# Optimization experiments

Hardware: AMD Instinct MI355X
Metric: run time of the kernel (lower is better)

## Reference

```python
import jax, jax.numpy as jnp
import numpy as np

NUM_HEADS = 4
HEAD_DIM = 64
IN_CH = 192
KERNEL_SIZES = (3, 5, 7, 9)  # per-head neighborhood size
NEG_INF = -1e30


def setup_inputs() -> dict:
    key = jax.random.key(0)
    k1, k2, k3 = jax.random.split(key, 3)
    x = jax.random.normal(k1, (8, IN_CH, 96, 96), dtype=jnp.float32)
    # QKV conv: out_channels = head_dim * num_heads * 3 = 768, 3x3, pad 1
    w_qkv = jax.random.normal(k2, (HEAD_DIM * NUM_HEADS * 3, IN_CH, 3, 3), dtype=jnp.float32) * 0.02
    b_qkv = jax.random.normal(k3, (HEAD_DIM * NUM_HEADS * 3,), dtype=jnp.float32) * 0.02
    return {"x": x, "w_qkv": w_qkv, "b_qkv": b_qkv}


def _neighborhood_attention(q, k, v, ksize):
    # q, k, v: [N, H, W, D]; KxK zero-padded neighborhood attention with
    # out-of-bounds positions masked out.
    N, H, W, D = q.shape
    pad = ksize // 2
    kp = jnp.pad(k, ((0, 0), (pad, pad), (pad, pad), (0, 0)))
    vp = jnp.pad(v, ((0, 0), (pad, pad), (pad, pad), (0, 0)))
    scale = 1.0 / np.sqrt(D).astype(np.float32)
    rows = jnp.arange(H)
    cols = jnp.arange(W)
    scores, masks = [], []
    for di in range(ksize):
        for dj in range(ksize):
            k_sh = kp[:, di:di + H, dj:dj + W, :]           # shifted keys
            scores.append(jnp.einsum('nhwd,nhwd->nhw', q, k_sh))
            rv = (rows + di - pad >= 0) & (rows + di - pad < H)   # [H]
            cv = (cols + dj - pad >= 0) & (cols + dj - pad < W)   # [W]
            masks.append(rv[:, None] & cv[None, :])               # [H, W]
    scores = jnp.stack(scores, axis=-1) * scale                   # [N,H,W,K2]
    mask = jnp.stack(masks, axis=-1)[None]                        # [1,H,W,K2]
    scores = jnp.where(mask, scores, NEG_INF)
    attn = jax.nn.softmax(scores, axis=-1)                        # [N,H,W,K2]
    out = jnp.zeros_like(q)
    t = 0
    for di in range(ksize):
        for dj in range(ksize):
            out = out + attn[..., t, None] * vp[:, di:di + H, dj:dj + W, :]
            t += 1
    return out  # [N,H,W,D]


def reference(x, w_qkv, b_qkv):
    # Dense QKV projection (Conv2d, stride 1, padding 1 == SAME for k=3)
    qkv = jax.lax.conv_general_dilated(
        x, w_qkv, window_strides=(1, 1), padding='SAME',
        dimension_numbers=('NCHW', 'OIHW', 'NCHW'))
    qkv = qkv + b_qkv[None, :, None, None]
    # transform_to_nhw1c: NCHW -> NHWC, then split channels into
    # num_heads blocks of 3*head_dim, each split into q, k, v.
    N, C, H, W = qkv.shape
    qkv = jnp.transpose(qkv, (0, 2, 3, 1)).reshape(N, H, W, NUM_HEADS, 3, HEAD_DIM)
    outs = []
    for h, ks in enumerate(KERNEL_SIZES):
        q = qkv[..., h, 0, :]
        k = qkv[..., h, 1, :]
        v = qkv[..., h, 2, :]
        o = _neighborhood_attention(q, k, v, ks)       # [N,H,W,D]
        outs.append(jnp.transpose(o, (0, 3, 1, 2)))    # transform_from_nhw1c -> NCHW
    return jnp.stack(outs, axis=0)  # [num_heads, N, D, H, W]
```

## Files before the change

kernel.cpp:

```cpp
#include <hip/hip_runtime.h>
#include <hip/hip_bf16.h>

#define NH 96
#define NW 96
#define NB 8
#define CIN 192
#define COUT 768
#define PH 98

typedef __attribute__((ext_vector_type(8))) unsigned short ushort8;
typedef __attribute__((ext_vector_type(8))) short bf16x8;
typedef __attribute__((ext_vector_type(4))) float f32x4;

static __device__ __forceinline__ unsigned short f2bf(float f) {
    unsigned int u = __float_as_uint(f);
    return (unsigned short)((u + 0x7fffu + ((u >> 16) & 1u)) >> 16);
}

typedef const __attribute__((address_space(1))) unsigned int gu32;
typedef __attribute__((address_space(3))) unsigned int lu32;
static __device__ __forceinline__ void gload16(const void* g, void* l) {
    __builtin_amdgcn_global_load_lds((gu32*)g, (lu32*)l, 16, 0, 0);
}

__global__ __launch_bounds__(256) void pack_x_kernel(
    const float* __restrict__ x, unsigned short* __restrict__ xp)
{
    __shared__ float tile[32][97];
    int bid = blockIdx.x;
    int ct = bid % 6; int y = (bid / 6) % NH; int n = bid / (6 * NH);
    int tid = threadIdx.x;
    int c0 = ct * 32;
    for (int i = tid; i < 32 * 96; i += 256) {
        int c = i / 96, xx = i % 96;
        tile[c][xx] = x[(((size_t)n * CIN + c0 + c) * NH + y) * NW + xx];
    }
    __syncthreads();
    for (int i = tid; i < 96 * 4; i += 256) {
        int xx = i >> 2, ch = i & 3;
        ushort8 pk;
#pragma unroll
        for (int j = 0; j < 8; ++j) pk[j] = f2bf(tile[ch * 8 + j][xx]);
        *(ushort8*)(xp + ((size_t)(n * PH + y + 1) * PH + xx + 1) * CIN + c0 + ch * 8) = pk;
    }
}

__global__ __launch_bounds__(256) void pack_w_kernel(
    const float* __restrict__ w, unsigned short* __restrict__ bw)
{
    __shared__ float ls[1728];
    int co = blockIdx.x; int tid = threadIdx.x;
    for (int i = tid; i < 1728; i += 256) ls[i] = w[(size_t)co * 1728 + i];
    __syncthreads();
    for (int i = tid; i < 1728; i += 256) {
        int sh = i / 192, ci = i % 192;
        bw[(size_t)co * 1728 + i] = f2bf(ls[ci * 9 + sh]);
    }
}

#define STAGE(S, BUF)                                                          \
    {                                                                          \
        int shift_ = (S) / 6, kk_ = (S) - shift_ * 6;                          \
        int aO_ = ((shift_ / 3) * PH + (shift_ % 3)) * CIN + kk_ * 32;         \
        int bO_ = (S) * 32;                                                    \
        _Pragma("unroll")                                                      \
        for (int i_ = 0; i_ < 2; ++i_) {                                       \
            gload16(srcA[i_] + aO_, dstA[i_] + (BUF));                         \
            gload16(srcB[i_] + bO_, dstB[i_] + (BUF));                         \
        }                                                                      \
    }

#define COMPUTE(CUR)                                                           \
    {                                                                          \
        bf16x8 af[8], bf[4];                                                   \
        _Pragma("unroll")                                                      \
        for (int m_ = 0; m_ < 8; ++m_)                                         \
            af[m_] = *(const bf16x8*)(smem + (CUR) + aoff[m_]);                \
        _Pragma("unroll")                                                      \
        for (int n_ = 0; n_ < 4; ++n_)                                         \
            bf[n_] = *(const bf16x8*)(smem + (CUR) + boff[n_]);                \
        __builtin_amdgcn_s_setprio(1);                                         \
        _Pragma("unroll")                                                      \
        for (int m_ = 0; m_ < 8; ++m_)                                         \
            _Pragma("unroll")                                                  \
            for (int n_ = 0; n_ < 4; ++n_)                                     \
                acc[m_][n_] = __builtin_amdgcn_mfma_f32_16x16x32_bf16(         \
                    af[m_], bf[n_], acc[m_][n_], 0, 0, 0);                     \
        __builtin_amdgcn_s_setprio(0);                                         \
    }

__global__ __launch_bounds__(512, 2) void conv_gemm_kernel(
    const unsigned short* __restrict__ xp, const unsigned short* __restrict__ bw,
    const float* __restrict__ bias, unsigned short* __restrict__ qkq,
    unsigned short* __restrict__ vt)
{
    __shared__ __align__(16) char smem[131072];
    int bid = (blockIdx.x & 7) * 108 + (blockIdx.x >> 3);
    int brow = (bid / 3) * 256, bcol = (bid % 3) * 256;
    int tid = threadIdx.x, lane = tid & 63, wid = tid >> 6;
    int wm = wid >> 2, wn = wid & 3;

    const unsigned short* srcA[2];
    const unsigned short* srcB[2];
    char* dstA[2];
    char* dstB[2];
#pragma unroll
    for (int i = 0; i < 2; ++i) {
        int s = i * 512 + tid;
        int row = s >> 2, c = s & 3;
        int p = brow + row;
        int n = p / 9216; int rem = p - n * 9216;
        int y = rem / 96; int xx = rem - y * 96;
        int csw = (c ^ ((row >> 1) & 3)) << 3;
        srcA[i] = xp + ((size_t)(n * PH + y) * PH + xx) * CIN + csw;
        srcB[i] = bw + (size_t)(bcol + row) * 1728 + csw;
        int uslot = i * 512 + (tid & ~63);
        dstA[i] = smem + uslot * 16;
        dstB[i] = smem + 16384 + uslot * 16;
    }

    int aoff[8], boff[4];
#pragma unroll
    for (int m = 0; m < 8; ++m) {
        int rowA = wm * 128 + m * 16 + (lane & 15);
        aoff[m] = rowA * 64 + (((lane >> 4) ^ ((rowA >> 1) & 3)) << 4);
    }
#pragma unroll
    for (int n = 0; n < 4; ++n) {
        int colB = wn * 64 + n * 16 + (lane & 15);
        boff[n] = 16384 + colB * 64 + (((lane >> 4) ^ ((colB >> 1) & 3)) << 4);
    }

    STAGE(0, 0);
    STAGE(1, 32768);
    STAGE(2, 65536);

    f32x4 acc[8][4] = {};

    for (int t = 0; t < 52; ++t) {
        asm volatile("s_waitcnt vmcnt(8)" ::: "memory");
        __builtin_amdgcn_s_barrier();
        if (t < 51) STAGE(t + 3, ((t + 3) & 3) << 15);
        __builtin_amdgcn_sched_barrier(0);
        COMPUTE((t & 3) << 15);
    }
    asm volatile("s_waitcnt vmcnt(4)" ::: "memory");
    __builtin_amdgcn_s_barrier();
    COMPUTE((52 & 3) << 15);
    asm volatile("s_waitcnt vmcnt(0)" ::: "memory");
    __builtin_amdgcn_s_barrier();
    COMPUTE((53 & 3) << 15);

    __syncthreads();
    unsigned short* sc = (unsigned short*)smem;
    float bn[4];
#pragma unroll
    for (int n = 0; n < 4; ++n)
        bn[n] = bias[bcol + wn * 64 + n * 16 + (lane & 15)];
#pragma unroll
    for (int m = 0; m < 8; ++m)
#pragma unroll
        for (int n = 0; n < 4; ++n) {
            int col = wn * 64 + n * 16 + (lane & 15);
            int cabs = bcol + col;
            float scale = ((cabs % 192) < 64) ? 0.125f : 1.0f;
#pragma unroll
            for (int j = 0; j < 4; ++j) {
                int row = wm * 128 + m * 16 + (lane >> 4) * 4 + j;
                sc[row * 256 + (col ^ ((row & 7) << 3))] =
                    f2bf((acc[m][n][j] + bn[n]) * scale);
            }
        }
    __syncthreads();
#pragma unroll
    for (int i = 0; i < 16; ++i) {
        int idx = i * 512 + tid;
        int row = idx >> 5, ch = idx & 31;
        int c0 = bcol + ch * 8;
        int r192 = c0 % 192;
        if (r192 < 128) {
            ushort8 pk = *(const ushort8*)(sc + row * 256 + ((ch * 8) ^ ((row & 7) << 3)));
            *(ushort8*)(qkq + (size_t)(brow + row) * 512 + (c0 / 192) * 128 + r192) = pk;
        }
    }
    int nblk = brow / 9216;
    int prem = brow - nblk * 9216;
#pragma unroll
    for (int h = 0; h < 4; ++h) {
        int lc = h * 192 + 128 - bcol;
        if (lc < 0 || lc > 192) continue;
        unsigned short* vth = vt + (size_t)h * 4718592;
#pragma unroll
        for (int it = 0; it < 4; ++it) {
            int i = it * 512 + tid;
            int d = i & 63, pxb = i >> 6;
            ushort8 pk;
#pragma unroll
            for (int j = 0; j < 8; ++j) {
                int px = pxb * 8 + j;
                pk[j] = sc[px * 256 + ((lc + d) ^ ((px & 7) << 3))];
            }
            *(ushort8*)(vth + ((size_t)(nblk * 64 + d)) * 9216 + prem + pxb * 8) = pk;
        }
    }
}

template<int KS>
static __device__ __forceinline__ void na_body(
    const unsigned short* __restrict__ qkq, const unsigned short* __restrict__ vt,
    float* __restrict__ out, int head, int bid)
{
    constexpr int PAD = KS / 2;
    __shared__ float sO[64][97];
    int y = bid % 96, n = bid / 96;
    int tid = threadIdx.x;
    int wv = tid >> 6, lane = tid & 63;
    int g = lane >> 4, pix = lane & 15;
    int x0 = wv * 16;
    int x = x0 + pix;
    int W = x0 - 8;

    size_t qbase = ((size_t)((n * 96 + y) * 96 + x)) * 512 + (size_t)head * 128;
    bf16x8 qf0 = *(const bf16x8*)(qkq + qbase + g * 8);
    bf16x8 qf1 = *(const bf16x8*)(qkq + qbase + 32 + g * 8);

    f32x4 s[KS][2];
#pragma unroll
    for (int di = 0; di < KS; ++di)
#pragma unroll
        for (int kt = 0; kt < 2; ++kt)
#pragma unroll
            for (int r = 0; r < 4; ++r) s[di][kt][r] = -1e30f;

#pragma unroll
    for (int di = 0; di < KS; ++di) {
        int iy = y + di - PAD;
        if (iy < 0 || iy >= 96) continue;
#pragma unroll
        for (int kt = 0; kt < 2; ++kt) {
            int kix_l = W + kt * 16 + pix;
            int ixc = min(max(kix_l, 0), 95);
            size_t kbase = ((size_t)((n * 96 + iy) * 96 + ixc)) * 512
                           + (size_t)head * 128 + 64;
            bf16x8 kf0 = *(const bf16x8*)(qkq + kbase + g * 8);
            bf16x8 kf1 = *(const bf16x8*)(qkq + kbase + 32 + g * 8);
            f32x4 t = {};
            t = __builtin_amdgcn_mfma_f32_16x16x32_bf16(kf0, qf0, t, 0, 0, 0);
            t = __builtin_amdgcn_mfma_f32_16x16x32_bf16(kf1, qf1, t, 0, 0, 0);
#pragma unroll
            for (int r = 0; r < 4; ++r) {
                int kix = W + kt * 16 + g * 4 + r;
                bool valid = ((unsigned)(kix - x + PAD) <= (unsigned)(2 * PAD)) &&
                             ((unsigned)kix < 96u);
                s[di][kt][r] = valid ? t[r] : -1e30f;
            }
        }
    }

    float m = -3.0e38f;
#pragma unroll
    for (int di = 0; di < KS; ++di)
#pragma unroll
        for (int kt = 0; kt < 2; ++kt)
#pragma unroll
            for (int r = 0; r < 4; ++r) m = fmaxf(m, s[di][kt][r]);
    m = fmaxf(m, __shfl_xor(m, 16, 64));
    m = fmaxf(m, __shfl_xor(m, 32, 64));
    float l = 0.f;
#pragma unroll
    for (int di = 0; di < KS; ++di)
#pragma unroll
        for (int kt = 0; kt < 2; ++kt)
#pragma unroll
            for (int r = 0; r < 4; ++r) {
                float p = __expf(s[di][kt][r] - m);
                s[di][kt][r] = p;
                l += p;
            }
    l += __shfl_xor(l, 16, 64);
    l += __shfl_xor(l, 32, 64);

    f32x4 O[4] = {};
    int addrA = ((2 * (g & 1)) * 16 + pix) * 4;
    int addrB = addrA + 64;
    bool kthi = (g >> 1) != 0;
#pragma unroll
    for (int di = 0; di < KS; ++di) {
        int iy = y + di - PAD;
        if (iy < 0 || iy >= 96) continue;
        unsigned int w0[2], w1[2];
#pragma unroll
        for (int kt = 0; kt < 2; ++kt) {
            asm("v_cvt_pk_bf16_f32 %0, %1, %2"
                : "=v"(w0[kt]) : "v"(s[di][kt][0]), "v"(s[di][kt][1]));
            asm("v_cvt_pk_bf16_f32 %0, %1, %2"
                : "=v"(w1[kt]) : "v"(s[di][kt][2]), "v"(s[di][kt][3]));
        }
        int a0 = __builtin_amdgcn_ds_bpermute(addrA, (int)w0[0]);
        int b0 = __builtin_amdgcn_ds_bpermute(addrA, (int)w0[1]);
        int a1 = __builtin_amdgcn_ds_bpermute(addrA, (int)w1[0]);
        int b1 = __builtin_amdgcn_ds_bpermute(addrA, (int)w1[1]);
        int a2 = __builtin_amdgcn_ds_bpermute(addrB, (int)w0[0]);
        int b2 = __builtin_amdgcn_ds_bpermute(addrB, (int)w0[1]);
        int a3 = __builtin_amdgcn_ds_bpermute(addrB, (int)w1[0]);
        int b3 = __builtin_amdgcn_ds_bpermute(addrB, (int)w1[1]);
        union { int u[4]; bf16x8 v; } pa;
        pa.u[0] = kthi ? b0 : a0;
        pa.u[1] = kthi ? b1 : a1;
        pa.u[2] = kthi ? b2 : a2;
        pa.u[3] = kthi ? b3 : a3;
#pragma unroll
        for (int dc = 0; dc < 4; ++dc) {
            long voff = ((long)((n * 64 + dc * 16 + pix) * 96 + iy)) * 96 + (W + g * 8);
            bf16x8 vf = *(const bf16x8*)(vt + voff);
            O[dc] = __builtin_amdgcn_mfma_f32_16x16x32_bf16(pa.v, vf, O[dc], 0, 0, 0);
        }
    }

    float linv = 1.0f / l;
    float linvj[4];
#pragma unroll
    for (int j = 0; j < 4; ++j)
        linvj[j] = __uint_as_float((unsigned)__builtin_amdgcn_ds_bpermute(
            (4 * g + j) * 4, (int)__float_as_uint(linv)));
#pragma unroll
    for (int dc = 0; dc < 4; ++dc)
#pragma unroll
        for (int j = 0; j < 4; ++j)
            sO[dc * 16 + pix][x0 + g * 4 + j] = O[dc][j] * linvj[j];
    __syncthreads();
    for (int i = tid; i < 1536; i += 384) {
        int d = i / 24, xq = i % 24;
        float4 v4 = { sO[d][xq * 4], sO[d][xq * 4 + 1],
                      sO[d][xq * 4 + 2], sO[d][xq * 4 + 3] };
        *(float4*)(out + ((size_t)(head * 8 + n) * 64 + d) * 9216
                   + y * 96 + xq * 4) = v4;
    }
}

__global__ __launch_bounds__(384, 3) void na_mfma_all(
    const unsigned short* __restrict__ qkq, const unsigned short* __restrict__ vt,
    float* __restrict__ out)
{
    int head = blockIdx.x / 768;
    int bid = blockIdx.x % 768;
    switch (head) {
        case 0: na_body<3>(qkq, vt,               out, 0, bid); break;
        case 1: na_body<5>(qkq, vt + 4718592,     out, 1, bid); break;
        case 2: na_body<7>(qkq, vt + 2 * 4718592, out, 2, bid); break;
        default: na_body<9>(qkq, vt + 3 * 4718592, out, 3, bid); break;
    }
}

extern "C" void kernel_launch(void* const* d_in, const int* in_sizes, int n_in,
                              void* d_out, int out_size, void* d_ws, size_t ws_size,
                              hipStream_t stream) {
    const float* x  = (const float*)d_in[0];
    const float* w  = (const float*)d_in[1];
    const float* b  = (const float*)d_in[2];
    float* out = (float*)d_out;

    unsigned short* qkq  = (unsigned short*)d_ws;
    unsigned short* vt   = (unsigned short*)((char*)d_ws + 75497472);
    unsigned short* xpad = (unsigned short*)((char*)d_ws + 113246208);
    unsigned short* bw   = (unsigned short*)((char*)d_ws + 142749696);

    hipMemsetAsync(xpad, 0, 29503488, stream);
    pack_x_kernel<<<NB * NH * 6, 256, 0, stream>>>(x, xpad);
    pack_w_kernel<<<COUT, 256, 0, stream>>>(w, bw);
    conv_gemm_kernel<<<864, 512, 0, stream>>>(xpad, bw, b, qkq, vt);

    na_mfma_all<<<4 * 768, 384, 0, stream>>>(qkq, vt, out);
}
```

Before: 373.5 us.

## Interleave LDS reads, global prefetch and MFMA in two phases per k-step

Splits the GEMM main loop body into two halves. Each half issues LDS fragment reads and half of the next stage's global_load_lds copies, then runs MFMAs under raised wave priority (s_setprio), with barriers separating the phases. The aim is to keep memory traffic and matrix-core work overlapped across waves in a ping-pong schedule. It adds extra barriers per iteration, which may cost synchronisation time if the waves do not settle into alternating phases.

```diff
diff --git a/kernel.cpp b/kernel.cpp
--- a/kernel.cpp
+++ b/kernel.cpp
@@ -140,9 +140,51 @@
     for (int t = 0; t < 52; ++t) {
         asm volatile("s_waitcnt vmcnt(8)" ::: "memory");
         __builtin_amdgcn_s_barrier();
-        if (t < 51) STAGE(t + 3, ((t + 3) & 3) << 15);
-        __builtin_amdgcn_sched_barrier(0);
-        COMPUTE((t & 3) << 15);
+        const int cur = (t & 3) << 15;
+        bf16x8 af[8], bf[4];
+#pragma unroll
+        for (int m_ = 0; m_ < 4; ++m_) af[m_] = *(const bf16x8*)(smem + cur + aoff[m_]);
+#pragma unroll
+        for (int n_ = 0; n_ < 4; ++n_) bf[n_] = *(const bf16x8*)(smem + cur + boff[n_]);
+        if (t < 51) {
+            int S = t + 3, BUF = (S & 3) << 15;
+            int shift_ = S / 6, kk_ = S - shift_ * 6;
+            int aO_ = ((shift_ / 3) * PH + (shift_ % 3)) * CIN + kk_ * 32;
+            gload16(srcA[0] + aO_, dstA[0] + BUF);
+            gload16(srcA[1] + aO_, dstA[1] + BUF);
+        }
+        asm volatile("" ::: "memory");
+        __builtin_amdgcn_s_barrier();
+        __builtin_amdgcn_s_setprio(1);
+#pragma unroll
+        for (int m_ = 0; m_ < 4; ++m_)
+#pragma unroll
+            for (int n_ = 0; n_ < 4; ++n_)
+                acc[m_][n_] = __builtin_amdgcn_mfma_f32_16x16x32_bf16(
+                    af[m_], bf[n_], acc[m_][n_], 0, 0, 0);
+        __builtin_amdgcn_s_setprio(0);
+        asm volatile("" ::: "memory");
+        __builtin_amdgcn_s_barrier();
+#pragma unroll
+        for (int m_ = 4; m_ < 8; ++m_) af[m_] = *(const bf16x8*)(smem + cur + aoff[m_]);
+        if (t < 51) {
+            int S = t + 3, BUF = (S & 3) << 15;
+            int bO_ = S * 32;
+            gload16(srcB[0] + bO_, dstB[0] + BUF);
+            gload16(srcB[1] + bO_, dstB[1] + BUF);
+        }
+        asm volatile("" ::: "memory");
+        __builtin_amdgcn_s_barrier();
+        __builtin_amdgcn_s_setprio(1);
+#pragma unroll
+        for (int m_ = 4; m_ < 8; ++m_)
+#pragma unroll
+            for (int n_ = 0; n_ < 4; ++n_)
+                acc[m_][n_] = __builtin_amdgcn_mfma_f32_16x16x32_bf16(
+                    af[m_], bf[n_], acc[m_][n_], 0, 0, 0);
+        __builtin_amdgcn_s_setprio(0);
+        asm volatile("" ::: "memory");
+        __builtin_amdgcn_s_barrier();
     }
     asm volatile("s_waitcnt vmcnt(4)" ::: "memory");
     __builtin_amdgcn_s_barrier();
```

New measurement: 379.5 us. No clear change (+1.6%).
